# Performance work log

Measured on AMD Instinct MI355X. Metric: run time of the kernel, lower is better.

Reference implementation:

```python
import jax, jax.numpy as jnp
import numpy as np

GRAPH_SIZE = 1024
D_MODEL = 256
BATCH = 32
INITIAL_ALPHA = 1.0


def setup_inputs() -> dict:
    key = jax.random.key(0)
    ks = jax.random.split(key, 10)
    s = 1.0 / np.sqrt(D_MODEL)  # torch Linear default init scale
    inp = {
        "query": jax.random.normal(ks[0], (BATCH, GRAPH_SIZE, D_MODEL), jnp.float32),
        "key_": jax.random.normal(ks[1], (BATCH, GRAPH_SIZE, D_MODEL), jnp.float32),
        "value": jax.random.normal(ks[2], (BATCH, GRAPH_SIZE, D_MODEL), jnp.float32),
        "dist": jax.random.uniform(ks[3], (BATCH, GRAPH_SIZE, GRAPH_SIZE), jnp.float32),
        "Wq": jax.random.uniform(ks[4], (D_MODEL, D_MODEL), jnp.float32, -s, s),
        "bq": jax.random.uniform(ks[5], (D_MODEL,), jnp.float32, -s, s),
        "Wk": jax.random.uniform(ks[6], (D_MODEL, D_MODEL), jnp.float32, -s, s),
        "bk": jax.random.uniform(ks[7], (D_MODEL,), jnp.float32, -s, s),
        "Wv": jax.random.uniform(ks[8], (D_MODEL, D_MODEL), jnp.float32, -s, s),
        "bv": jax.random.uniform(ks[9], (D_MODEL,), jnp.float32, -s, s),
        # alpha_raw = exp(initial_alpha - 1)
        "alpha_raw": jnp.asarray(np.exp(INITIAL_ALPHA - 1.0), jnp.float32),
    }
    return inp


def reference(query, key_, value, dist, Wq, bq, Wk, bk, Wv, bv, alpha_raw):
    # self-attention path: mask=None, cross=False, query_size == graph_size
    log2_N = jnp.log2(jnp.asarray(GRAPH_SIZE, jnp.float32))
    alpha = jax.nn.softplus(alpha_raw) + 1e-6

    q = jnp.einsum('bnd,ed->bne', query, Wq) + bq   # fc_q
    k = jnp.einsum('bnd,ed->bne', key_, Wk) + bk    # fc_k
    v = jnp.einsum('bnd,ed->bne', value, Wv) + bv   # fc_v

    exp_A = jnp.exp(-alpha * log2_N * dist)         # [b, n, n]
    exp_K = jnp.exp(k)                              # [b, n, d]

    numerator = jnp.einsum('bqk,bkd->bqd', exp_A, exp_K * v)
    denominator = jnp.einsum('bqk,bkd->bqd', exp_A, exp_K) + 1e-8
    return jax.nn.sigmoid(q) * (numerator / denominator)
```

## Files before the change

kernel.cpp:

```cpp
#include <hip/hip_runtime.h>
#include <hip/hip_bf16.h>

#define NBATCH 32
#define NG 1024
#define DM 256
#define HB 16

typedef short bf16x8 __attribute__((ext_vector_type(8)));
typedef float f32x4 __attribute__((ext_vector_type(4)));
typedef unsigned short u16x4 __attribute__((ext_vector_type(4)));
typedef unsigned short u16x8 __attribute__((ext_vector_type(8)));

static __device__ __forceinline__ unsigned short f2bf(float f) {
    __hip_bfloat16 h = __float2bfloat16(f);
    return *reinterpret_cast<unsigned short*>(&h);
}

static __device__ __forceinline__ void gload16(const void* g, void* l) {
    __builtin_amdgcn_global_load_lds(
        (const __attribute__((address_space(1))) unsigned int*)g,
        (__attribute__((address_space(3))) unsigned int*)l, 16, 0, 0);
}

static __device__ __forceinline__ void gemm_tile(
    const float* __restrict__ Xrow, const float* __restrict__ Wt,
    int tid, f32x4 (&acc)[2][4],
    unsigned short* lds_a, unsigned short* lds_w)
{
    const int lane = tid & 63, wv = tid >> 6;
    const int l15 = lane & 15, lhi = lane >> 4;
    const int arow = tid >> 1, ac0 = (tid & 1) << 5;
    const int wrow = tid >> 2, wc0 = (tid & 3) << 4;

    #pragma unroll
    for (int mi = 0; mi < 2; ++mi)
        #pragma unroll
        for (int ni = 0; ni < 4; ++ni)
            acc[mi][ni] = (f32x4){0.f, 0.f, 0.f, 0.f};

    for (int ks = 0; ks < 4; ++ks) {
        const float* asrc = Xrow + (size_t)arow * DM + ks * 64 + ac0;
        #pragma unroll
        for (int j = 0; j < 8; ++j) {
            float4 v = *(const float4*)(asrc + 4 * j);
            u16x4 p = { f2bf(v.x), f2bf(v.y), f2bf(v.z), f2bf(v.w) };
            *(u16x4*)&lds_a[arow * 72 + ac0 + 4 * j] = p;
        }
        const float* wsrc = Wt + (size_t)wrow * DM + ks * 64 + wc0;
        #pragma unroll
        for (int j = 0; j < 4; ++j) {
            float4 v = *(const float4*)(wsrc + 4 * j);
            u16x4 p = { f2bf(v.x), f2bf(v.y), f2bf(v.z), f2bf(v.w) };
            *(u16x4*)&lds_w[wrow * 72 + wc0 + 4 * j] = p;
        }
        __syncthreads();
        #pragma unroll
        for (int kk = 0; kk < 2; ++kk) {
            const int kb = kk * 32 + lhi * 8;
            bf16x8 bfr[4];
            #pragma unroll
            for (int ni = 0; ni < 4; ++ni)
                bfr[ni] = *(const bf16x8*)&lds_w[(ni * 16 + l15) * 72 + kb];
            #pragma unroll
            for (int mi = 0; mi < 2; ++mi) {
                bf16x8 af = *(const bf16x8*)&lds_a[(wv * 32 + mi * 16 + l15) * 72 + kb];
                #pragma unroll
                for (int ni = 0; ni < 4; ++ni)
                    acc[mi][ni] = __builtin_amdgcn_mfma_f32_16x16x32_bf16(
                        af, bfr[ni], acc[mi][ni], 0, 0, 0);
            }
        }
        __syncthreads();
    }
}

__global__ __launch_bounds__(256) void proj_kernel(
    const float* __restrict__ query, const float* __restrict__ key_,
    const float* __restrict__ value,
    const float* __restrict__ Wq, const float* __restrict__ bq,
    const float* __restrict__ Wk, const float* __restrict__ bk,
    const float* __restrict__ Wv, const float* __restrict__ bv,
    float* __restrict__ sigq, unsigned short* __restrict__ Pt)
{
    __shared__ unsigned short lds_a[128 * 72];
    __shared__ unsigned short lds_w[64 * 72];

    const int bid = blockIdx.x;
    const int b  = bid >> 5;
    const int kt = (bid >> 2) & 7;
    const int dt = bid & 3;
    const int tid = threadIdx.x;
    const int w = tid >> 6, lane = tid & 63;
    const int l15 = lane & 15, lhi = lane >> 4;

    const float* xq = query + ((size_t)b * NG + kt * 128) * DM;
    const float* xk = key_  + ((size_t)b * NG + kt * 128) * DM;
    const float* xv = value + ((size_t)b * NG + kt * 128) * DM;

    f32x4 aq[2][4];
    gemm_tile(xq, Wq + dt * 64 * DM, tid, aq, lds_a, lds_w);
    #pragma unroll
    for (int mi = 0; mi < 2; ++mi)
        #pragma unroll
        for (int ni = 0; ni < 4; ++ni) {
            const int colg = dt * 64 + ni * 16 + l15;
            const float bqs = bq[colg];
            #pragma unroll
            for (int r = 0; r < 4; ++r) {
                const int nrow = kt * 128 + w * 32 + mi * 16 + lhi * 4 + r;
                const float qv = aq[mi][ni][r] + bqs;
                sigq[((size_t)b * NG + nrow) * DM + colg] = 1.0f / (1.0f + __expf(-qv));
            }
        }

    f32x4 ak[2][4], av[2][4];
    gemm_tile(xk, Wk + dt * 64 * DM, tid, ak, lds_a, lds_w);
    gemm_tile(xv, Wv + dt * 64 * DM, tid, av, lds_a, lds_w);

    #pragma unroll
    for (int mi = 0; mi < 2; ++mi)
        #pragma unroll
        for (int ni = 0; ni < 4; ++ni) {
            const int colg = dt * 64 + ni * 16 + l15;
            const float bks = bk[colg], bvs = bv[colg];
            unsigned short p1[4], p2[4];
            #pragma unroll
            for (int r = 0; r < 4; ++r) {
                const float ek = __expf(ak[mi][ni][r] + bks);
                const float vv = av[mi][ni][r] + bvs;
                p1[r] = f2bf(ek * vv);
                p2[r] = f2bf(ek);
            }
            const int kk0 = kt * 128 + w * 32 + mi * 16 + lhi * 4;
            *(u16x4*)&Pt[((size_t)b * 512 + 2 * colg    ) * NG + kk0] =
                (u16x4){p1[0], p1[1], p1[2], p1[3]};
            *(u16x4*)&Pt[((size_t)b * 512 + 2 * colg + 1) * NG + kk0] =
                (u16x4){p2[0], p2[1], p2[2], p2[3]};
        }
}

__global__ __launch_bounds__(256) void exp_kernel(
    const float* __restrict__ dist, unsigned short* __restrict__ ea,
    const float* __restrict__ alpha_raw)
{
    const float alpha = log1pf(__expf(alpha_raw[0])) + 1e-6f;
    const float sc = -alpha * 10.0f * 1.44269504088896f;
    const size_t i8 = ((size_t)blockIdx.x * 256 + threadIdx.x) * 8;
    float4 v0 = *(const float4*)(dist + i8);
    float4 v1 = *(const float4*)(dist + i8 + 4);
    u16x8 o = { f2bf(exp2f(sc * v0.x)), f2bf(exp2f(sc * v0.y)),
                f2bf(exp2f(sc * v0.z)), f2bf(exp2f(sc * v0.w)),
                f2bf(exp2f(sc * v1.x)), f2bf(exp2f(sc * v1.y)),
                f2bf(exp2f(sc * v1.z)), f2bf(exp2f(sc * v1.w)) };
    *(u16x8*)(ea + i8) = o;
}

__global__ __launch_bounds__(256) void attn_kernel(
    const unsigned short* __restrict__ ea,
    const unsigned short* __restrict__ Pt,
    float* __restrict__ out)
{
    __shared__ __align__(128) unsigned short lds[2][2][128 * 64];

    const int bid = blockIdx.x;
    const int l = (bid & 7) * 64 + (bid >> 3);
    const int b = l >> 5;
    const int m = (l >> 2) & 7;
    const int n = l & 3;

    const int tid = threadIdx.x;
    const int w = tid >> 6, lane = tid & 63;
    const int wm = w >> 1, wn = w & 1;
    const int l15 = lane & 15, lhi = lane >> 4;
    const int lr = lane >> 3, cb = lane & 7;
    const int cbs = cb ^ lr;

    const char* Abase = (const char*)(ea + ((size_t)b * NG + m * 128) * NG);
    const char* Bbase = (const char*)(Pt + ((size_t)b * 512 + n * 128) * NG);

    f32x4 acc[4][4];
    #pragma unroll
    for (int mi = 0; mi < 4; ++mi)
        #pragma unroll
        for (int ni = 0; ni < 4; ++ni)
            acc[mi][ni] = (f32x4){0.f, 0.f, 0.f, 0.f};

    auto STAGE = [&](int buf, int t) {
        #pragma unroll
        for (int i = 0; i < 4; ++i) {
            const int r = w * 32 + i * 8 + lr;
            const size_t goff = (size_t)r * 2048 + t * 128 + cbs * 16;
            char* ldst = (char*)&lds[buf][0][0] + w * 4096 + i * 1024;
            gload16(Abase + goff, ldst);
            gload16(Bbase + goff, ldst + 16384);
        }
    };

    STAGE(0, 0);
    __syncthreads();

    int cur = 0;
    for (int t = 0; t < 16; ++t) {
        if (t < 15) STAGE(cur ^ 1, t + 1);
        const char* Ab = (const char*)&lds[cur][0][0];
        const char* Bb = (const char*)&lds[cur][1][0];
        #pragma unroll
        for (int kk = 0; kk < 2; ++kk) {
            const int bc = kk * 64 + lhi * 16;
            bf16x8 af[4], bfr[4];
            #pragma unroll
            for (int mi = 0; mi < 4; ++mi) {
                const int tr = wm * 64 + mi * 16 + l15;
                af[mi] = *(const bf16x8*)(Ab + ((tr * 128 + bc) ^ ((tr & 7) << 4)));
            }
            #pragma unroll
            for (int ni = 0; ni < 4; ++ni) {
                const int tr = wn * 64 + ni * 16 + l15;
                bfr[ni] = *(const bf16x8*)(Bb + ((tr * 128 + bc) ^ ((tr & 7) << 4)));
            }
            #pragma unroll
            for (int mi = 0; mi < 4; ++mi)
                #pragma unroll
                for (int ni = 0; ni < 4; ++ni)
                    acc[mi][ni] = __builtin_amdgcn_mfma_f32_16x16x32_bf16(
                        af[mi], bfr[ni], acc[mi][ni], 0, 0, 0);
        }
        __syncthreads();
        cur ^= 1;
    }

    const int parity = lane & 1;
    #pragma unroll
    for (int mi = 0; mi < 4; ++mi)
        #pragma unroll
        for (int ni = 0; ni < 4; ++ni)
            #pragma unroll
            for (int r = 0; r < 4; ++r) {
                const float own = acc[mi][ni][r];
                const float other = __shfl_xor(own, 1, 64);
                if (!parity) {
                    const int colg = n * 128 + wn * 64 + ni * 16 + l15;
                    const int d = colg >> 1;
                    const int rowg = m * 128 + wm * 64 + mi * 16 + lhi * 4 + r;
                    const size_t idx = ((size_t)b * NG + rowg) * DM + d;
                    out[idx] = out[idx] * (own / (other + 1e-8f));
                }
            }
}

extern "C" void kernel_launch(void* const* d_in, const int* in_sizes, int n_in,
                              void* d_out, int out_size, void* d_ws, size_t ws_size,
                              hipStream_t stream) {
    const float* query = (const float*)d_in[0];
    const float* key_  = (const float*)d_in[1];
    const float* value = (const float*)d_in[2];
    const float* dist  = (const float*)d_in[3];
    const float* Wq = (const float*)d_in[4];
    const float* bq = (const float*)d_in[5];
    const float* Wk = (const float*)d_in[6];
    const float* bk = (const float*)d_in[7];
    const float* Wv = (const float*)d_in[8];
    const float* bv = (const float*)d_in[9];
    const float* alpha_raw = (const float*)d_in[10];
    float* out = (float*)d_out;

    unsigned short* Pt = (unsigned short*)d_ws;
    unsigned short* exp_buf =
        (unsigned short*)((char*)d_ws + (size_t)NBATCH * 512 * NG * sizeof(unsigned short));

    proj_kernel<<<dim3(1024), dim3(256), 0, stream>>>(
        query, key_, value, Wq, bq, Wk, bk, Wv, bv, out, Pt);

    for (int h = 0; h < 2; ++h) {
        exp_kernel<<<dim3(8192), dim3(256), 0, stream>>>(
            dist + (size_t)h * HB * NG * NG, exp_buf, alpha_raw);
        attn_kernel<<<dim3(512), dim3(256), 0, stream>>>(
            exp_buf, Pt + (size_t)h * HB * 512 * NG, out + (size_t)h * HB * NG * DM);
    }
}
```

Before: 206.5 us.

## Restructure projection kernel to load each input tile once with double-buffered LDS

Each projection block now covers 64 rows and all 256 output columns, so every row of query/key/value is read from global memory once instead of four times. The bf16 input tile goes to LDS, double-buffered, and the next input is prefetched into registers while the current GEMM runs. Weight fragments are read straight from global/L2 and converted in registers, with no LDS staging. The grid is halved, and register pressure rises from the 4x4 accumulators and the 16-float4 prefetch buffers.

```diff
diff --git a/kernel.cpp b/kernel.cpp
--- a/kernel.cpp
+++ b/kernel.cpp
@@ -22,56 +22,13 @@
         (__attribute__((address_space(3))) unsigned int*)l, 16, 0, 0);
 }
 
-static __device__ __forceinline__ void gemm_tile(
-    const float* __restrict__ Xrow, const float* __restrict__ Wt,
-    int tid, f32x4 (&acc)[2][4],
-    unsigned short* lds_a, unsigned short* lds_w)
-{
-    const int lane = tid & 63, wv = tid >> 6;
-    const int l15 = lane & 15, lhi = lane >> 4;
-    const int arow = tid >> 1, ac0 = (tid & 1) << 5;
-    const int wrow = tid >> 2, wc0 = (tid & 3) << 4;
-
-    #pragma unroll
-    for (int mi = 0; mi < 2; ++mi)
-        #pragma unroll
-        for (int ni = 0; ni < 4; ++ni)
-            acc[mi][ni] = (f32x4){0.f, 0.f, 0.f, 0.f};
-
-    for (int ks = 0; ks < 4; ++ks) {
-        const float* asrc = Xrow + (size_t)arow * DM + ks * 64 + ac0;
-        #pragma unroll
-        for (int j = 0; j < 8; ++j) {
-            float4 v = *(const float4*)(asrc + 4 * j);
-            u16x4 p = { f2bf(v.x), f2bf(v.y), f2bf(v.z), f2bf(v.w) };
-            *(u16x4*)&lds_a[arow * 72 + ac0 + 4 * j] = p;
-        }
-        const float* wsrc = Wt + (size_t)wrow * DM + ks * 64 + wc0;
-        #pragma unroll
-        for (int j = 0; j < 4; ++j) {
-            float4 v = *(const float4*)(wsrc + 4 * j);
-            u16x4 p = { f2bf(v.x), f2bf(v.y), f2bf(v.z), f2bf(v.w) };
-            *(u16x4*)&lds_w[wrow * 72 + wc0 + 4 * j] = p;
-        }
-        __syncthreads();
-        #pragma unroll
-        for (int kk = 0; kk < 2; ++kk) {
-            const int kb = kk * 32 + lhi * 8;
-            bf16x8 bfr[4];
-            #pragma unroll
-            for (int ni = 0; ni < 4; ++ni)
-                bfr[ni] = *(const bf16x8*)&lds_w[(ni * 16 + l15) * 72 + kb];
-            #pragma unroll
-            for (int mi = 0; mi < 2; ++mi) {
-                bf16x8 af = *(const bf16x8*)&lds_a[(wv * 32 + mi * 16 + l15) * 72 + kb];
-                #pragma unroll
-                for (int ni = 0; ni < 4; ++ni)
-                    acc[mi][ni] = __builtin_amdgcn_mfma_f32_16x16x32_bf16(
-                        af, bfr[ni], acc[mi][ni], 0, 0, 0);
-            }
-        }
-        __syncthreads();
-    }
+static __device__ __forceinline__ bf16x8 ldW(const float* p) {
+    float4 a = *(const float4*)p;
+    float4 b = *(const float4*)(p + 4);
+    union { u16x8 u; bf16x8 h; } t;
+    t.u = (u16x8){ f2bf(a.x), f2bf(a.y), f2bf(a.z), f2bf(a.w),
+                   f2bf(b.x), f2bf(b.y), f2bf(b.z), f2bf(b.w) };
+    return t.h;
 }
 
 __global__ __launch_bounds__(256) void proj_kernel(
@@ -82,47 +39,108 @@
     const float* __restrict__ Wv, const float* __restrict__ bv,
     float* __restrict__ sigq, unsigned short* __restrict__ Pt)
 {
-    __shared__ unsigned short lds_a[128 * 72];
-    __shared__ unsigned short lds_w[64 * 72];
+    __shared__ unsigned short xa[2][64 * 264];
 
     const int bid = blockIdx.x;
-    const int b  = bid >> 5;
-    const int kt = (bid >> 2) & 7;
-    const int dt = bid & 3;
+    const int b = bid >> 4, rt = bid & 15;
     const int tid = threadIdx.x;
     const int w = tid >> 6, lane = tid & 63;
     const int l15 = lane & 15, lhi = lane >> 4;
 
-    const float* xq = query + ((size_t)b * NG + kt * 128) * DM;
-    const float* xk = key_  + ((size_t)b * NG + kt * 128) * DM;
-    const float* xv = value + ((size_t)b * NG + kt * 128) * DM;
-
-    f32x4 aq[2][4];
-    gemm_tile(xq, Wq + dt * 64 * DM, tid, aq, lds_a, lds_w);
-    #pragma unroll
-    for (int mi = 0; mi < 2; ++mi)
+    const int sr = tid >> 2;
+    const int sc = (tid & 3) << 6;
+
+    const size_t xoff = ((size_t)b * NG + rt * 64) * DM + (size_t)sr * DM + sc;
+    const float* xq = query + xoff;
+    const float* xk = key_  + xoff;
+    const float* xv = value + xoff;
+
+    auto GEMM = [&](const unsigned short* xbuf, const float* Wf, f32x4 (&acc)[4][4]) {
+        #pragma unroll
+        for (int mi = 0; mi < 4; ++mi)
+            #pragma unroll
+            for (int ni = 0; ni < 4; ++ni)
+                acc[mi][ni] = (f32x4){0.f, 0.f, 0.f, 0.f};
+        #pragma unroll
+        for (int kk = 0; kk < 8; ++kk) {
+            bf16x8 bfr[4], af[4];
+            #pragma unroll
+            for (int ni = 0; ni < 4; ++ni)
+                bfr[ni] = ldW(Wf + (size_t)((w * 64 + ni * 16 + l15) << 8) + kk * 32 + lhi * 8);
+            #pragma unroll
+            for (int mi = 0; mi < 4; ++mi)
+                af[mi] = *(const bf16x8*)&xbuf[(mi * 16 + l15) * 264 + kk * 32 + lhi * 8];
+            #pragma unroll
+            for (int mi = 0; mi < 4; ++mi)
+                #pragma unroll
+                for (int ni = 0; ni < 4; ++ni)
+                    acc[mi][ni] = __builtin_amdgcn_mfma_f32_16x16x32_bf16(
+                        af[mi], bfr[ni], acc[mi][ni], 0, 0, 0);
+        }
+    };
+
+    {
+        float4 t[16];
+        #pragma unroll
+        for (int j = 0; j < 16; ++j) t[j] = *(const float4*)(xq + 4 * j);
+        #pragma unroll
+        for (int j = 0; j < 16; ++j) {
+            u16x4 p = { f2bf(t[j].x), f2bf(t[j].y), f2bf(t[j].z), f2bf(t[j].w) };
+            *(u16x4*)&xa[0][sr * 264 + sc + 4 * j] = p;
+        }
+    }
+    __syncthreads();
+
+    float4 tk[16];
+    #pragma unroll
+    for (int j = 0; j < 16; ++j) tk[j] = *(const float4*)(xk + 4 * j);
+
+    {
+        f32x4 aq[4][4];
+        GEMM(&xa[0][0], Wq, aq);
+        #pragma unroll
+        for (int j = 0; j < 16; ++j) {
+            u16x4 p = { f2bf(tk[j].x), f2bf(tk[j].y), f2bf(tk[j].z), f2bf(tk[j].w) };
+            *(u16x4*)&xa[1][sr * 264 + sc + 4 * j] = p;
+        }
         #pragma unroll
         for (int ni = 0; ni < 4; ++ni) {
-            const int colg = dt * 64 + ni * 16 + l15;
+            const int colg = w * 64 + ni * 16 + l15;
             const float bqs = bq[colg];
             #pragma unroll
-            for (int r = 0; r < 4; ++r) {
-                const int nrow = kt * 128 + w * 32 + mi * 16 + lhi * 4 + r;
-                const float qv = aq[mi][ni][r] + bqs;
-                sigq[((size_t)b * NG + nrow) * DM + colg] = 1.0f / (1.0f + __expf(-qv));
-            }
-        }
-
-    f32x4 ak[2][4], av[2][4];
-    gemm_tile(xk, Wk + dt * 64 * DM, tid, ak, lds_a, lds_w);
-    gemm_tile(xv, Wv + dt * 64 * DM, tid, av, lds_a, lds_w);
-
-    #pragma unroll
-    for (int mi = 0; mi < 2; ++mi)
-        #pragma unroll
-        for (int ni = 0; ni < 4; ++ni) {
-            const int colg = dt * 64 + ni * 16 + l15;
-            const float bks = bk[colg], bvs = bv[colg];
+            for (int mi = 0; mi < 4; ++mi)
+                #pragma unroll
+                for (int r = 0; r < 4; ++r) {
+                    const int rowg = rt * 64 + mi * 16 + lhi * 4 + r;
+                    const float qv = aq[mi][ni][r] + bqs;
+                    sigq[((size_t)b * NG + rowg) * DM + colg] = 1.0f / (1.0f + __expf(-qv));
+                }
+        }
+    }
+    __syncthreads();
+
+    float4 tv[16];
+    #pragma unroll
+    for (int j = 0; j < 16; ++j) tv[j] = *(const float4*)(xv + 4 * j);
+
+    f32x4 ak[4][4];
+    GEMM(&xa[1][0], Wk, ak);
+    #pragma unroll
+    for (int j = 0; j < 16; ++j) {
+        u16x4 p = { f2bf(tv[j].x), f2bf(tv[j].y), f2bf(tv[j].z), f2bf(tv[j].w) };
+        *(u16x4*)&xa[0][sr * 264 + sc + 4 * j] = p;
+    }
+    __syncthreads();
+
+    f32x4 av[4][4];
+    GEMM(&xa[0][0], Wv, av);
+
+    #pragma unroll
+    for (int ni = 0; ni < 4; ++ni) {
+        const int colg = w * 64 + ni * 16 + l15;
+        const float bks = bk[colg], bvs = bv[colg];
+        #pragma unroll
+        for (int mi = 0; mi < 4; ++mi) {
             unsigned short p1[4], p2[4];
             #pragma unroll
             for (int r = 0; r < 4; ++r) {
@@ -131,12 +149,13 @@
                 p1[r] = f2bf(ek * vv);
                 p2[r] = f2bf(ek);
             }
-            const int kk0 = kt * 128 + w * 32 + mi * 16 + lhi * 4;
+            const int kk0 = rt * 64 + mi * 16 + lhi * 4;
             *(u16x4*)&Pt[((size_t)b * 512 + 2 * colg    ) * NG + kk0] =
                 (u16x4){p1[0], p1[1], p1[2], p1[3]};
             *(u16x4*)&Pt[((size_t)b * 512 + 2 * colg + 1) * NG + kk0] =
                 (u16x4){p2[0], p2[1], p2[2], p2[3]};
         }
+    }
 }
 
 __global__ __launch_bounds__(256) void exp_kernel(
@@ -268,7 +287,7 @@
     unsigned short* exp_buf =
         (unsigned short*)((char*)d_ws + (size_t)NBATCH * 512 * NG * sizeof(unsigned short));
 
-    proj_kernel<<<dim3(1024), dim3(256), 0, stream>>>(
+    proj_kernel<<<dim3(512), dim3(256), 0, stream>>>(
         query, key_, value, Wq, bq, Wk, bk, Wv, bv, out, Pt);
 
     for (int h = 0; h < 2; ++h) {
```

Result: no change. 203.3 us (-1.5%).

## Pre-pack weights to bf16 and restructure projection to skip LDS staging

Applied to the files above, without the earlier changes.

Adds a small kernel that converts Wq/Wk/Wv to bf16 once into workspace. The projection kernel is retiled so each block covers 32 rows by all 256 output columns, with each wave owning 64 columns. MFMA operands are now loaded straight from global memory into registers instead of being staged through LDS with barriers. This removes the per-tile fp32-to-bf16 weight conversion and the LDS synchronisation, but depends on cache hits for the weights and for X rows that all four waves reload.

```diff
diff --git a/kernel.cpp b/kernel.cpp
--- a/kernel.cpp
+++ b/kernel.cpp
@@ -22,107 +22,94 @@
         (__attribute__((address_space(3))) unsigned int*)l, 16, 0, 0);
 }
 
-static __device__ __forceinline__ void gemm_tile(
-    const float* __restrict__ Xrow, const float* __restrict__ Wt,
-    int tid, f32x4 (&acc)[2][4],
-    unsigned short* lds_a, unsigned short* lds_w)
-{
-    const int lane = tid & 63, wv = tid >> 6;
+static __device__ __forceinline__ bf16x8 pack8(const float* p) {
+    float4 a = *(const float4*)p;
+    float4 b = *(const float4*)(p + 4);
+    union { u16x8 u; bf16x8 h; } t;
+    t.u = (u16x8){ f2bf(a.x), f2bf(a.y), f2bf(a.z), f2bf(a.w),
+                   f2bf(b.x), f2bf(b.y), f2bf(b.z), f2bf(b.w) };
+    return t.h;
+}
+
+__global__ __launch_bounds__(256) void wpack_kernel(
+    const float* __restrict__ Wq, const float* __restrict__ Wk,
+    const float* __restrict__ Wv, unsigned short* __restrict__ Wb)
+{
+    const int i4 = (blockIdx.x * 256 + threadIdx.x) * 4;
+    const int t = i4 >> 16;
+    const int off = i4 & 65535;
+    const float* src = (t == 0) ? Wq : (t == 1) ? Wk : Wv;
+    float4 v = *(const float4*)(src + off);
+    *(u16x4*)(Wb + i4) = (u16x4){ f2bf(v.x), f2bf(v.y), f2bf(v.z), f2bf(v.w) };
+}
+
+__global__ __launch_bounds__(256) void proj_kernel(
+    const float* __restrict__ query, const float* __restrict__ key_,
+    const float* __restrict__ value,
+    const unsigned short* __restrict__ Wb,
+    const float* __restrict__ bq, const float* __restrict__ bk,
+    const float* __restrict__ bv,
+    float* __restrict__ sigq, unsigned short* __restrict__ Pt)
+{
+    const int bid = blockIdx.x;
+    const int b = bid >> 5, rt = bid & 31;
+    const int tid = threadIdx.x;
+    const int w = tid >> 6, lane = tid & 63;
     const int l15 = lane & 15, lhi = lane >> 4;
-    const int arow = tid >> 1, ac0 = (tid & 1) << 5;
-    const int wrow = tid >> 2, wc0 = (tid & 3) << 4;
-
-    #pragma unroll
-    for (int mi = 0; mi < 2; ++mi)
-        #pragma unroll
-        for (int ni = 0; ni < 4; ++ni)
-            acc[mi][ni] = (f32x4){0.f, 0.f, 0.f, 0.f};
-
-    for (int ks = 0; ks < 4; ++ks) {
-        const float* asrc = Xrow + (size_t)arow * DM + ks * 64 + ac0;
-        #pragma unroll
-        for (int j = 0; j < 8; ++j) {
-            float4 v = *(const float4*)(asrc + 4 * j);
-            u16x4 p = { f2bf(v.x), f2bf(v.y), f2bf(v.z), f2bf(v.w) };
-            *(u16x4*)&lds_a[arow * 72 + ac0 + 4 * j] = p;
-        }
-        const float* wsrc = Wt + (size_t)wrow * DM + ks * 64 + wc0;
-        #pragma unroll
-        for (int j = 0; j < 4; ++j) {
-            float4 v = *(const float4*)(wsrc + 4 * j);
-            u16x4 p = { f2bf(v.x), f2bf(v.y), f2bf(v.z), f2bf(v.w) };
-            *(u16x4*)&lds_w[wrow * 72 + wc0 + 4 * j] = p;
-        }
-        __syncthreads();
-        #pragma unroll
-        for (int kk = 0; kk < 2; ++kk) {
-            const int kb = kk * 32 + lhi * 8;
-            bf16x8 bfr[4];
+
+    const size_t xbase = ((size_t)b * NG + rt * 32) * DM;
+
+    auto GEMMX = [&](const float* __restrict__ X, const unsigned short* __restrict__ Wf,
+                     f32x4 (&acc)[2][4]) {
+        #pragma unroll
+        for (int mi = 0; mi < 2; ++mi)
             #pragma unroll
             for (int ni = 0; ni < 4; ++ni)
-                bfr[ni] = *(const bf16x8*)&lds_w[(ni * 16 + l15) * 72 + kb];
-            #pragma unroll
-            for (int mi = 0; mi < 2; ++mi) {
-                bf16x8 af = *(const bf16x8*)&lds_a[(wv * 32 + mi * 16 + l15) * 72 + kb];
+                acc[mi][ni] = (f32x4){0.f, 0.f, 0.f, 0.f};
+        #pragma unroll
+        for (int kk = 0; kk < 8; ++kk) {
+            bf16x8 af[2], bfr[4];
+            #pragma unroll
+            for (int mi = 0; mi < 2; ++mi)
+                af[mi] = pack8(X + xbase + (size_t)(mi * 16 + l15) * DM + kk * 32 + lhi * 8);
+            #pragma unroll
+            for (int ni = 0; ni < 4; ++ni)
+                bfr[ni] = *(const bf16x8*)&Wf[((w * 64 + ni * 16 + l15) << 8) + kk * 32 + lhi * 8];
+            #pragma unroll
+            for (int mi = 0; mi < 2; ++mi)
                 #pragma unroll
                 for (int ni = 0; ni < 4; ++ni)
                     acc[mi][ni] = __builtin_amdgcn_mfma_f32_16x16x32_bf16(
-                        af, bfr[ni], acc[mi][ni], 0, 0, 0);
-            }
-        }
-        __syncthreads();
-    }
-}
-
-__global__ __launch_bounds__(256) void proj_kernel(
-    const float* __restrict__ query, const float* __restrict__ key_,
-    const float* __restrict__ value,
-    const float* __restrict__ Wq, const float* __restrict__ bq,
-    const float* __restrict__ Wk, const float* __restrict__ bk,
-    const float* __restrict__ Wv, const float* __restrict__ bv,
-    float* __restrict__ sigq, unsigned short* __restrict__ Pt)
-{
-    __shared__ unsigned short lds_a[128 * 72];
-    __shared__ unsigned short lds_w[64 * 72];
-
-    const int bid = blockIdx.x;
-    const int b  = bid >> 5;
-    const int kt = (bid >> 2) & 7;
-    const int dt = bid & 3;
-    const int tid = threadIdx.x;
-    const int w = tid >> 6, lane = tid & 63;
-    const int l15 = lane & 15, lhi = lane >> 4;
-
-    const float* xq = query + ((size_t)b * NG + kt * 128) * DM;
-    const float* xk = key_  + ((size_t)b * NG + kt * 128) * DM;
-    const float* xv = value + ((size_t)b * NG + kt * 128) * DM;
+                        af[mi], bfr[ni], acc[mi][ni], 0, 0, 0);
+        }
+    };
 
     f32x4 aq[2][4];
-    gemm_tile(xq, Wq + dt * 64 * DM, tid, aq, lds_a, lds_w);
-    #pragma unroll
-    for (int mi = 0; mi < 2; ++mi)
-        #pragma unroll
-        for (int ni = 0; ni < 4; ++ni) {
-            const int colg = dt * 64 + ni * 16 + l15;
-            const float bqs = bq[colg];
+    GEMMX(query, Wb, aq);
+    #pragma unroll
+    for (int ni = 0; ni < 4; ++ni) {
+        const int colg = w * 64 + ni * 16 + l15;
+        const float bqs = bq[colg];
+        #pragma unroll
+        for (int mi = 0; mi < 2; ++mi)
             #pragma unroll
             for (int r = 0; r < 4; ++r) {
-                const int nrow = kt * 128 + w * 32 + mi * 16 + lhi * 4 + r;
+                const int rowg = rt * 32 + mi * 16 + lhi * 4 + r;
                 const float qv = aq[mi][ni][r] + bqs;
-                sigq[((size_t)b * NG + nrow) * DM + colg] = 1.0f / (1.0f + __expf(-qv));
-            }
-        }
+                sigq[((size_t)b * NG + rowg) * DM + colg] = 1.0f / (1.0f + __expf(-qv));
+            }
+    }
 
     f32x4 ak[2][4], av[2][4];
-    gemm_tile(xk, Wk + dt * 64 * DM, tid, ak, lds_a, lds_w);
-    gemm_tile(xv, Wv + dt * 64 * DM, tid, av, lds_a, lds_w);
-
-    #pragma unroll
-    for (int mi = 0; mi < 2; ++mi)
-        #pragma unroll
-        for (int ni = 0; ni < 4; ++ni) {
-            const int colg = dt * 64 + ni * 16 + l15;
-            const float bks = bk[colg], bvs = bv[colg];
+    GEMMX(key_,  Wb + 65536,  ak);
+    GEMMX(value, Wb + 131072, av);
+
+    #pragma unroll
+    for (int ni = 0; ni < 4; ++ni) {
+        const int colg = w * 64 + ni * 16 + l15;
+        const float bks = bk[colg], bvs = bv[colg];
+        #pragma unroll
+        for (int mi = 0; mi < 2; ++mi) {
             unsigned short p1[4], p2[4];
             #pragma unroll
             for (int r = 0; r < 4; ++r) {
@@ -131,12 +118,13 @@
                 p1[r] = f2bf(ek * vv);
                 p2[r] = f2bf(ek);
             }
-            const int kk0 = kt * 128 + w * 32 + mi * 16 + lhi * 4;
+            const int kk0 = rt * 32 + mi * 16 + lhi * 4;
             *(u16x4*)&Pt[((size_t)b * 512 + 2 * colg    ) * NG + kk0] =
                 (u16x4){p1[0], p1[1], p1[2], p1[3]};
             *(u16x4*)&Pt[((size_t)b * 512 + 2 * colg + 1) * NG + kk0] =
                 (u16x4){p2[0], p2[1], p2[2], p2[3]};
         }
+    }
 }
 
 __global__ __launch_bounds__(256) void exp_kernel(
@@ -267,9 +255,12 @@
     unsigned short* Pt = (unsigned short*)d_ws;
     unsigned short* exp_buf =
         (unsigned short*)((char*)d_ws + (size_t)NBATCH * 512 * NG * sizeof(unsigned short));
+    unsigned short* Wb = exp_buf + (size_t)HB * NG * NG;
+
+    wpack_kernel<<<dim3(192), dim3(256), 0, stream>>>(Wq, Wk, Wv, Wb);
 
     proj_kernel<<<dim3(1024), dim3(256), 0, stream>>>(
-        query, key_, value, Wq, bq, Wk, bk, Wv, bv, out, Pt);
+        query, key_, value, Wb, bq, bk, bv, out, Pt);
 
     for (int h = 0; h < 2; ++h) {
         exp_kernel<<<dim3(8192), dim3(256), 0, stream>>>(
```

After: 253.8 us. 22.9% more time.
